# Kernel optimization log

Measured on AMD Instinct MI355X. Metric: run time of the kernel, lower is better.

Reference implementation:

```python
import jax, jax.numpy as jnp
import numpy as np

# Structure constants C[i, j, k] for the Cl(3,0) geometric product with basis
# order [1, e1, e2, e3, e12, e13, e23, e123]: (a*b)_k = sum_ij a_i b_j C[i,j,k].
_TABLE = [
    (0,0,0,1),(1,1,0,1),(2,2,0,1),(3,3,0,1),(4,4,0,-1),(5,5,0,-1),(6,6,0,-1),(7,7,0,-1),
    (0,1,1,1),(1,0,1,1),(2,4,1,-1),(4,2,1,1),(3,5,1,-1),(5,3,1,1),(6,7,1,-1),(7,6,1,-1),
    (0,2,2,1),(2,0,2,1),(1,4,2,1),(4,1,2,-1),(3,6,2,-1),(6,3,2,1),(5,7,2,1),(7,5,2,1),
    (0,3,3,1),(3,0,3,1),(1,5,3,1),(5,1,3,-1),(2,6,3,1),(6,2,3,-1),(4,7,3,-1),(7,4,3,-1),
    (0,4,4,1),(4,0,4,1),(1,2,4,1),(2,1,4,-1),(3,7,4,1),(7,3,4,1),(5,6,4,-1),(6,5,4,1),
    (0,5,5,1),(5,0,5,1),(1,3,5,1),(3,1,5,-1),(2,7,5,-1),(7,2,5,-1),(4,6,5,1),(6,4,5,-1),
    (0,6,6,1),(6,0,6,1),(2,3,6,1),(3,2,6,-1),(1,7,6,1),(7,1,6,1),(4,5,6,-1),(5,4,6,1),
    (0,7,7,1),(7,0,7,1),(1,6,7,1),(6,1,7,1),(2,5,7,-1),(5,2,7,-1),(3,4,7,1),(4,3,7,1),
]
_C = np.zeros((8, 8, 8), dtype=np.float32)
for _i, _j, _k, _s in _TABLE:
    _C[_i, _j, _k] = _s

B, IN_F, OUT_F = 65536, 64, 64


def setup_inputs() -> dict:
    key = jax.random.key(0)
    ks = jax.random.split(key, 5)
    return {
        "x": jax.random.normal(ks[0], (B, IN_F, 8), dtype=jnp.float32),
        "weight": jax.random.normal(ks[1], (OUT_F, IN_F, 8), dtype=jnp.float32) * 0.02,
        "bias": jnp.zeros((OUT_F, 8), dtype=jnp.float32),
        "row_scale": jax.random.uniform(ks[2], (OUT_F,), dtype=jnp.float32),
        "col_scale": jax.random.uniform(ks[3], (IN_F,), dtype=jnp.float32),
        "bias_shift": jax.random.normal(ks[4], (OUT_F,), dtype=jnp.float32),
    }


def reference(x, weight, bias, row_scale, col_scale, bias_shift):
    C = jnp.asarray(_C)  # [8,8,8] structure constants
    w = weight * row_scale[:, None, None] * col_scale[None, :, None]
    w = jnp.nan_to_num(w, nan=0.0)
    # Fold structure constants into the (small) weight first: wc[o,n,i,k]
    wc = jnp.einsum('onj,ijk->onik', w, C)
    # out[b,o,k] = sum_{n,i} x[b,n,i] * wc[o,n,i,k]  (geometric product + sum over in)
    out = jnp.einsum('bni,onik->bok', x, wc)
    out = out + bias[None]
    out = out.at[..., 0].add(bias_shift[None, :])
    return out
```

## Files before the change

kernel.cpp:

```cpp
#include <hip/hip_runtime.h>
#include <cstdint>

#define M_DIM 65536
#define N_DIM 512
#define K_DIM 512
#define BM 128
#define BN 128
#define BK 32
#define KSTEPS (K_DIM / BK)

typedef float f32x4 __attribute__((ext_vector_type(4)));
typedef __bf16 bf16x8 __attribute__((ext_vector_type(8)));
typedef unsigned short us8 __attribute__((ext_vector_type(8)));

__device__ __forceinline__ unsigned short f2bf(float f) {
  unsigned int u = __builtin_bit_cast(unsigned int, f);
  u += 0x7fffu + ((u >> 16) & 1u);
  return (unsigned short)(u >> 16);
}

__device__ __forceinline__ unsigned int cvt_pk_bf16(float lo, float hi) {
  unsigned int r;
  asm("v_cvt_pk_bf16_f32 %0, %1, %2" : "=v"(r) : "v"(lo), "v"(hi));
  return r;
}

__global__ void clifford_prep(const float* __restrict__ weight,
                              const float* __restrict__ bias,
                              const float* __restrict__ row_scale,
                              const float* __restrict__ col_scale,
                              const float* __restrict__ bias_shift,
                              unsigned short* __restrict__ WCT2,
                              float* __restrict__ bias2) {
  const int t = blockIdx.x * 256 + threadIdx.x;
  if (t < 512) {
    const int o = t >> 3, k = t & 7;
    bias2[t] = bias[t] + (k == 0 ? bias_shift[o] : 0.0f);
  }
  if (t >= 64 * 64) return;
  const int o = t >> 6, n = t & 63;
  const float rs = row_scale[o], cs = col_scale[n];
  float w[8];
#pragma unroll
  for (int j = 0; j < 8; ++j) {
    float v = weight[(size_t)t * 8 + j] * rs * cs;
    w[j] = (v != v) ? 0.0f : v;
  }
  constexpr int TI[64] = {0,1,2,3,4,5,6,7, 0,1,2,4,3,5,6,7, 0,2,1,4,3,6,5,7,
                          0,3,1,5,2,6,4,7, 0,4,1,2,3,7,5,6, 0,5,1,3,2,7,4,6,
                          0,6,2,3,1,7,4,5, 0,7,1,6,2,5,3,4};
  constexpr int TJ[64] = {0,1,2,3,4,5,6,7, 1,0,4,2,5,3,7,6, 2,0,4,1,6,3,7,5,
                          3,0,5,1,6,2,7,4, 4,0,2,1,7,3,6,5, 5,0,3,1,7,2,6,4,
                          6,0,3,2,7,1,5,4, 7,0,6,1,5,2,4,3};
  constexpr int TK[64] = {0,0,0,0,0,0,0,0, 1,1,1,1,1,1,1,1, 2,2,2,2,2,2,2,2,
                          3,3,3,3,3,3,3,3, 4,4,4,4,4,4,4,4, 5,5,5,5,5,5,5,5,
                          6,6,6,6,6,6,6,6, 7,7,7,7,7,7,7,7};
  constexpr float TS[64] = {1,1,1,1,-1,-1,-1,-1, 1,1,-1,1,-1,1,-1,-1, 1,1,1,-1,-1,1,1,1,
                            1,1,1,-1,1,-1,-1,-1, 1,1,1,-1,1,1,-1,1,  1,1,1,-1,-1,-1,1,-1,
                            1,1,1,-1,1,1,-1,1,   1,1,1,1,-1,-1,1,1};
  float wc[8][8];
#pragma unroll
  for (int i = 0; i < 8; ++i)
#pragma unroll
    for (int k = 0; k < 8; ++k) wc[i][k] = 0.0f;
#pragma unroll
  for (int e = 0; e < 64; ++e) wc[TI[e]][TK[e]] += TS[e] * w[TJ[e]];
#pragma unroll
  for (int kb = 0; kb < 8; ++kb)
#pragma unroll
    for (int i = 0; i < 8; ++i)
      WCT2[((size_t)n * N_DIM + o * 8 + kb) * 8 + i] = f2bf(wc[i][kb]);
}

__global__ __launch_bounds__(256) void clifford_gemm(
    const float* __restrict__ x, const unsigned short* __restrict__ WCT2,
    const float* __restrict__ bias2, float* __restrict__ out) {
  __shared__ __align__(16) unsigned short As[2][BM * BK];

  const int tid = threadIdx.x;
  const int lane = tid & 63;
  const int wv = tid >> 6;

  const int bid = blockIdx.x;
  const int grp = bid >> 5, r = bid & 31;
  const size_t m0 = (size_t)(grp * 8 + (r & 7)) * BM;
  const int n0 = (r >> 3) * BN;

  const int s_row = tid >> 1;
  const int s_half = tid & 1;
  const float* ag = x + (m0 + s_row) * (size_t)K_DIM + s_half * 16;

  const int wm = (wv & 1) * 64;
  const int wn = (wv >> 1) * 64;
  const int lm = lane & 15;
  const int kg = lane >> 4;

  const unsigned short* bg = WCT2 + ((size_t)kg * N_DIM + (n0 + wn + lm)) * 8;

  f32x4 ar[4];
  const f32x4 zero = {0.f, 0.f, 0.f, 0.f};
  f32x4 acc[4][4];
#pragma unroll
  for (int i = 0; i < 4; ++i)
#pragma unroll
    for (int j = 0; j < 4; ++j) acc[i][j] = zero;

  auto loadA = [&](int kc) {
#pragma unroll
    for (int j = 0; j < 4; ++j) ar[j] = *(const f32x4*)(ag + kc + j * 4);
  };
  auto writeA = [&](int b) {
    union { us8 v; unsigned int w[4]; } p0, p1;
    p0.w[0] = cvt_pk_bf16(ar[0][0], ar[0][1]);
    p0.w[1] = cvt_pk_bf16(ar[0][2], ar[0][3]);
    p0.w[2] = cvt_pk_bf16(ar[1][0], ar[1][1]);
    p0.w[3] = cvt_pk_bf16(ar[1][2], ar[1][3]);
    p1.w[0] = cvt_pk_bf16(ar[2][0], ar[2][1]);
    p1.w[1] = cvt_pk_bf16(ar[2][2], ar[2][3]);
    p1.w[2] = cvt_pk_bf16(ar[3][0], ar[3][1]);
    p1.w[3] = cvt_pk_bf16(ar[3][2], ar[3][3]);
    unsigned short* d0 = &As[b][((s_half * 2) * BM + s_row) * 8];
    unsigned short* d1 = &As[b][((s_half * 2 + 1) * BM + s_row) * 8];
    *(us8*)d0 = p0.v;
    *(us8*)d1 = p1.v;
  };
  auto loadB = [&](us8 (&bb)[4], int ks) {
    const unsigned short* p = bg + (size_t)ks * (4 * N_DIM * 8);
#pragma unroll
    for (int ni = 0; ni < 4; ++ni) bb[ni] = *(const us8*)(p + ni * 128);
  };

  us8 b0[4], b1[4];

  loadA(0);
  writeA(0);
  loadB(b0, 0);
  __syncthreads();

  auto body = [&](int ks, int pb, us8 (&bc)[4], us8 (&bn)[4]) {
    const bool last = (ks == KSTEPS - 1);
    if (!last) {
      loadA((ks + 1) * BK);
      loadB(bn, ks + 1);
    }
    bf16x8 af[4];
#pragma unroll
    for (int mi = 0; mi < 4; ++mi)
      af[mi] = __builtin_bit_cast(
          bf16x8, *(const us8*)&As[pb][((size_t)kg * BM + wm + mi * 16 + lm) * 8]);
#pragma unroll
    for (int mi = 0; mi < 4; ++mi)
#pragma unroll
      for (int ni = 0; ni < 4; ++ni)
        acc[mi][ni] = __builtin_amdgcn_mfma_f32_16x16x32_bf16(
            af[mi], __builtin_bit_cast(bf16x8, bc[ni]), acc[mi][ni], 0, 0, 0);
    if (!last) {
      writeA(pb ^ 1);
      __syncthreads();
    }
  };

  for (int ks2 = 0; ks2 < KSTEPS; ks2 += 2) {
    body(ks2, 0, b0, b1);
    body(ks2 + 1, 1, b1, b0);
  }

#pragma unroll
  for (int ni = 0; ni < 4; ++ni) {
    const int nn = n0 + wn + ni * 16 + lm;
    const float b2 = bias2[nn];
#pragma unroll
    for (int mi = 0; mi < 4; ++mi) {
#pragma unroll
      for (int rr = 0; rr < 4; ++rr) {
        const size_t mm = m0 + wm + mi * 16 + kg * 4 + rr;
        out[mm * N_DIM + nn] = acc[mi][ni][rr] + b2;
      }
    }
  }
}

extern "C" void kernel_launch(void* const* d_in, const int* in_sizes, int n_in,
                              void* d_out, int out_size, void* d_ws, size_t ws_size,
                              hipStream_t stream) {
  const float* x          = (const float*)d_in[0];
  const float* weight     = (const float*)d_in[1];
  const float* bias       = (const float*)d_in[2];
  const float* row_scale  = (const float*)d_in[3];
  const float* col_scale  = (const float*)d_in[4];
  const float* bias_shift = (const float*)d_in[5];

  unsigned short* WCT2 = (unsigned short*)d_ws;
  float* bias2 = (float*)((char*)d_ws + (size_t)N_DIM * K_DIM * 2);

  clifford_prep<<<16, 256, 0, stream>>>(weight, bias, row_scale, col_scale,
                                        bias_shift, WCT2, bias2);
  clifford_gemm<<<(M_DIM / BM) * (N_DIM / BN), 256, 0, stream>>>(
      x, WCT2, bias2, (float*)d_out);
}
```

Before: 283.7 us.

## Load A fragments directly from global into registers, dropping LDS staging

```diff
diff --git a/kernel.cpp b/kernel.cpp
--- a/kernel.cpp
+++ b/kernel.cpp
@@ -17,12 +17,6 @@
   unsigned int u = __builtin_bit_cast(unsigned int, f);
   u += 0x7fffu + ((u >> 16) & 1u);
   return (unsigned short)(u >> 16);
-}
-
-__device__ __forceinline__ unsigned int cvt_pk_bf16(float lo, float hi) {
-  unsigned int r;
-  asm("v_cvt_pk_bf16_f32 %0, %1, %2" : "=v"(r) : "v"(lo), "v"(hi));
-  return r;
 }
 
 __global__ void clifford_prep(const float* __restrict__ weight,
@@ -72,11 +66,9 @@
       WCT2[((size_t)n * N_DIM + o * 8 + kb) * 8 + i] = f2bf(wc[i][kb]);
 }
 
-__global__ __launch_bounds__(256) void clifford_gemm(
+__global__ __launch_bounds__(256, 3) void clifford_gemm(
     const float* __restrict__ x, const unsigned short* __restrict__ WCT2,
     const float* __restrict__ bias2, float* __restrict__ out) {
-  __shared__ __align__(16) unsigned short As[2][BM * BK];
-
   const int tid = threadIdx.x;
   const int lane = tid & 63;
   const int wv = tid >> 6;
@@ -86,18 +78,18 @@
   const size_t m0 = (size_t)(grp * 8 + (r & 7)) * BM;
   const int n0 = (r >> 3) * BN;
 
-  const int s_row = tid >> 1;
-  const int s_half = tid & 1;
-  const float* ag = x + (m0 + s_row) * (size_t)K_DIM + s_half * 16;
-
   const int wm = (wv & 1) * 64;
   const int wn = (wv >> 1) * 64;
   const int lm = lane & 15;
   const int kg = lane >> 4;
 
+  const float* am[4];
+#pragma unroll
+  for (int mi = 0; mi < 4; ++mi)
+    am[mi] = x + (m0 + wm + mi * 16 + lm) * (size_t)K_DIM + kg * 8;
+
   const unsigned short* bg = WCT2 + ((size_t)kg * N_DIM + (n0 + wn + lm)) * 8;
 
-  f32x4 ar[4];
   const f32x4 zero = {0.f, 0.f, 0.f, 0.f};
   f32x4 acc[4][4];
 #pragma unroll
@@ -105,64 +97,55 @@
 #pragma unroll
     for (int j = 0; j < 4; ++j) acc[i][j] = zero;
 
-  auto loadA = [&](int kc) {
+  f32x4 a[4][2];
+  us8 b0[4], b1[4];
+
+  auto loadA = [&](int ks) {
 #pragma unroll
-    for (int j = 0; j < 4; ++j) ar[j] = *(const f32x4*)(ag + kc + j * 4);
-  };
-  auto writeA = [&](int b) {
-    union { us8 v; unsigned int w[4]; } p0, p1;
-    p0.w[0] = cvt_pk_bf16(ar[0][0], ar[0][1]);
-    p0.w[1] = cvt_pk_bf16(ar[0][2], ar[0][3]);
-    p0.w[2] = cvt_pk_bf16(ar[1][0], ar[1][1]);
-    p0.w[3] = cvt_pk_bf16(ar[1][2], ar[1][3]);
-    p1.w[0] = cvt_pk_bf16(ar[2][0], ar[2][1]);
-    p1.w[1] = cvt_pk_bf16(ar[2][2], ar[2][3]);
-    p1.w[2] = cvt_pk_bf16(ar[3][0], ar[3][1]);
-    p1.w[3] = cvt_pk_bf16(ar[3][2], ar[3][3]);
-    unsigned short* d0 = &As[b][((s_half * 2) * BM + s_row) * 8];
-    unsigned short* d1 = &As[b][((s_half * 2 + 1) * BM + s_row) * 8];
-    *(us8*)d0 = p0.v;
-    *(us8*)d1 = p1.v;
+    for (int mi = 0; mi < 4; ++mi) {
+      a[mi][0] = *(const f32x4*)(am[mi] + ks * BK);
+      a[mi][1] = *(const f32x4*)(am[mi] + ks * BK + 4);
+    }
   };
   auto loadB = [&](us8 (&bb)[4], int ks) {
     const unsigned short* p = bg + (size_t)ks * (4 * N_DIM * 8);
 #pragma unroll
     for (int ni = 0; ni < 4; ++ni) bb[ni] = *(const us8*)(p + ni * 128);
   };
-
-  us8 b0[4], b1[4];
+  auto cvtA = [&](bf16x8 (&af)[4]) {
+#pragma unroll
+    for (int mi = 0; mi < 4; ++mi) {
+      bf16x8 t;
+#pragma unroll
+      for (int j = 0; j < 4; ++j) {
+        t[j] = (__bf16)a[mi][0][j];
+        t[4 + j] = (__bf16)a[mi][1][j];
+      }
+      af[mi] = t;
+    }
+  };
 
   loadA(0);
-  writeA(0);
   loadB(b0, 0);
-  __syncthreads();
 
-  auto body = [&](int ks, int pb, us8 (&bc)[4], us8 (&bn)[4]) {
-    const bool last = (ks == KSTEPS - 1);
-    if (!last) {
-      loadA((ks + 1) * BK);
+  auto body = [&](int ks, us8 (&bc)[4], us8 (&bn)[4]) {
+    bf16x8 af[4];
+    cvtA(af);
+    if (ks < KSTEPS - 1) {
+      loadA(ks + 1);
       loadB(bn, ks + 1);
     }
-    bf16x8 af[4];
-#pragma unroll
-    for (int mi = 0; mi < 4; ++mi)
-      af[mi] = __builtin_bit_cast(
-          bf16x8, *(const us8*)&As[pb][((size_t)kg * BM + wm + mi * 16 + lm) * 8]);
 #pragma unroll
     for (int mi = 0; mi < 4; ++mi)
 #pragma unroll
       for (int ni = 0; ni < 4; ++ni)
         acc[mi][ni] = __builtin_amdgcn_mfma_f32_16x16x32_bf16(
             af[mi], __builtin_bit_cast(bf16x8, bc[ni]), acc[mi][ni], 0, 0, 0);
-    if (!last) {
-      writeA(pb ^ 1);
-      __syncthreads();
-    }
   };
 
   for (int ks2 = 0; ks2 < KSTEPS; ks2 += 2) {
-    body(ks2, 0, b0, b1);
-    body(ks2 + 1, 1, b1, b0);
+    body(ks2, b0, b1);
+    body(ks2 + 1, b1, b0);
   }
 
 #pragma unroll
```

Result: slower. 329.6 us (+16.2%).
